# Kernel tuning notes

Measured on AMD Instinct MI355X. Metric: run time of the kernel, lower is better.

Reference implementation:

```python
import jax, jax.numpy as jnp
import numpy as np

N = 100000        # nodes
E = 1600000       # directed edges (before self loops)
F = 128           # input node features
H1, H2, H3 = 64, 32, 16
G = 64            # graphs in batch
EPS = 1e-5
NEG_SLOPE = 0.2


def setup_inputs():
    key = jax.random.key(0)
    ks = jax.random.split(key, 16)
    def rn(k, shape, scale=1.0):
        return jax.random.normal(k, shape, dtype=jnp.float32) * scale
    inp = {}
    inp['x'] = rn(ks[0], (N, F))
    inp['edge_index'] = jax.random.randint(ks[1], (2, E), 0, N)
    inp['batch'] = jnp.sort(jax.random.randint(ks[2], (N,), 0, G))
    dims = [(F, H1), (H1, H2), (H2, H3)]
    i = 3
    for li, (fi, fo) in enumerate(dims, start=1):
        s = 1.0 / np.sqrt(fi)
        kk = jax.random.split(ks[i], 3)
        inp[f'Wl{li}'] = rn(kk[0], (fi, fo), s)
        inp[f'bl{li}'] = jnp.zeros((fo,), jnp.float32)
        inp[f'Wr{li}'] = rn(kk[1], (fi, fo), s)
        inp[f'br{li}'] = jnp.zeros((fo,), jnp.float32)
        inp[f'att{li}'] = rn(kk[2], (fo,), 1.0 / np.sqrt(fo))
        inp[f'bias{li}'] = jnp.zeros((fo,), jnp.float32)
        inp[f'gamma{li}'] = jnp.ones((fo,), jnp.float32)
        inp[f'beta{li}'] = jnp.zeros((fo,), jnp.float32)
        i += 1
    inp['linW'] = rn(ks[i], (H3, 1), 0.25)
    inp['linb'] = jnp.zeros((1,), jnp.float32)
    return inp


def _gatv2(x, Wl, bl, Wr, br, att, bias, src, dst):
    # PyG GATv2Conv, heads=1: e_ij = a^T LeakyReLU(Wl x_j + Wr x_i)
    xl = x @ Wl + bl                         # [N, H] source transform
    xr = x @ Wr + br                         # [N, H] target transform
    e = jax.nn.leaky_relu(xl[src] + xr[dst], NEG_SLOPE) @ att   # [E']
    # numerically stable segment softmax over incoming edges of dst
    emax = jax.ops.segment_max(e, dst, num_segments=N)
    w = jnp.exp(e - emax[dst])
    denom = jax.ops.segment_sum(w, dst, num_segments=N)
    alpha = w / (denom[dst] + 1e-16)         # [E']
    out = jax.ops.segment_sum(alpha[:, None] * xl[src], dst, num_segments=N)
    return out + bias


def _batchnorm(x, gamma, beta):
    mu = jnp.mean(x, axis=0)
    var = jnp.var(x, axis=0)
    return (x - mu) * jax.lax.rsqrt(var + EPS) * gamma + beta


def reference(x, edge_index, batch,
              Wl1, bl1, Wr1, br1, att1, bias1, gamma1, beta1,
              Wl2, bl2, Wr2, br2, att2, bias2, gamma2, beta2,
              Wl3, bl3, Wr3, br3, att3, bias3, gamma3, beta3,
              linW, linb):
    # add self loops once (PyG GATv2Conv default add_self_loops=True)
    loops = jnp.arange(N, dtype=edge_index.dtype)
    src = jnp.concatenate([edge_index[0], loops])
    dst = jnp.concatenate([edge_index[1], loops])

    h = _gatv2(x, Wl1, bl1, Wr1, br1, att1, bias1, src, dst)
    h = jax.nn.relu(_batchnorm(h, gamma1, beta1))
    h = _gatv2(h, Wl2, bl2, Wr2, br2, att2, bias2, src, dst)
    h = jax.nn.relu(_batchnorm(h, gamma2, beta2))
    h = _gatv2(h, Wl3, bl3, Wr3, br3, att3, bias3, src, dst)
    h = jax.nn.relu(_batchnorm(h, gamma3, beta3))

    # global mean pool over graphs
    sums = jax.ops.segment_sum(h, batch, num_segments=G)          # [G, 16]
    cnts = jax.ops.segment_sum(jnp.ones((N,), h.dtype), batch, num_segments=G)
    pooled = sums / jnp.maximum(cnts, 1.0)[:, None]
    return pooled @ linW + linb                                   # [G, 1]
```

## Files before the change

### kernel.cpp

```cpp
#include <hip/hip_runtime.h>
#include <hip/hip_bf16.h>


static constexpr int G_ = 64;

typedef short bfrag __attribute__((ext_vector_type(8)));
typedef float facc  __attribute__((ext_vector_type(4)));

__device__ __forceinline__ float asfloat_(unsigned int u) {
  union { unsigned int i; float f; } c; c.i = u; return c.f;
}
__device__ __forceinline__ float bf2f(unsigned short u) {
  return asfloat_(((unsigned int)u) << 16);
}
__device__ __forceinline__ unsigned short f2bf(float f) {
  union { float f; unsigned int i; } c;
  c.f = f;
  unsigned int r = c.i + 0x7FFFu + ((c.i >> 16) & 1u);
  return (unsigned short)(r >> 16);
}

template <int FPL>
__device__ __forceinline__ void load_bf(const unsigned short* p, float* f) {
  if constexpr (FPL == 8) {
    uint4 q = *reinterpret_cast<const uint4*>(p);
    f[0] = asfloat_(q.x << 16); f[1] = asfloat_(q.x & 0xFFFF0000u);
    f[2] = asfloat_(q.y << 16); f[3] = asfloat_(q.y & 0xFFFF0000u);
    f[4] = asfloat_(q.z << 16); f[5] = asfloat_(q.z & 0xFFFF0000u);
    f[6] = asfloat_(q.w << 16); f[7] = asfloat_(q.w & 0xFFFF0000u);
  } else {
    uint2 q = *reinterpret_cast<const uint2*>(p);
    f[0] = asfloat_(q.x << 16); f[1] = asfloat_(q.x & 0xFFFF0000u);
    f[2] = asfloat_(q.y << 16); f[3] = asfloat_(q.y & 0xFFFF0000u);
  }
}

__global__ __launch_bounds__(256) void pack_all(
    const float* __restrict__ Wl1, const float* __restrict__ Wr1,
    const float* __restrict__ bl1, const float* __restrict__ br1,
    const float* __restrict__ Wl2, const float* __restrict__ Wr2,
    const float* __restrict__ bl2, const float* __restrict__ br2,
    const float* __restrict__ Wl3, const float* __restrict__ Wr3,
    const float* __restrict__ bl3, const float* __restrict__ br3,
    unsigned short* __restrict__ Wt1, float* __restrict__ bc1,
    unsigned short* __restrict__ Wt2, float* __restrict__ bc2,
    unsigned short* __restrict__ Wt3, float* __restrict__ bc3) {
  int i = blockIdx.x * 256 + threadIdx.x;
  if (i < 128 * 128) { int c = i >> 7, k = i & 127;
    Wt1[i] = f2bf((c < 64) ? Wl1[k * 64 + c] : Wr1[k * 64 + (c - 64)]); }
  if (i < 128) bc1[i] = (i < 64) ? bl1[i] : br1[i - 64];
  if (i < 64 * 64) { int c = i >> 6, k = i & 63;
    Wt2[i] = f2bf((c < 32) ? Wl2[k * 32 + c] : Wr2[k * 32 + (c - 32)]); }
  if (i < 64) bc2[i] = (i < 32) ? bl2[i] : br2[i - 32];
  if (i < 32 * 32) { int c = i >> 5, k = i & 31;
    Wt3[i] = f2bf((c < 16) ? Wl3[k * 16 + c] : Wr3[k * 16 + (c - 16)]); }
  if (i < 32) bc3[i] = (i < 16) ? bl3[i] : br3[i - 16];
}

__global__ __launch_bounds__(256) void edge_hist(
    const int* __restrict__ ei, int* __restrict__ deg, int E, int Etot, int N) {
  int p = blockIdx.x & 7;
  int q = blockIdx.x >> 3;
  int nbq = gridDim.x >> 3;
  float scale = 8.0f / (float)N;
  for (int i = q * 256 + threadIdx.x; i < Etot; i += nbq * 256) {
    int dst = (i < E) ? ei[E + i] : (i - E);
    int pp = min((int)((float)dst * scale), 7);
    if (pp == p) atomicAdd(&deg[dst], 1);
  }
}

__global__ __launch_bounds__(256) void scan1(
    const int* __restrict__ deg, int* __restrict__ part, int* __restrict__ bsums, int n) {
  __shared__ int ts[256];
  int t = threadIdx.x, b = blockIdx.x;
  int base = b * 1024 + t * 4;
  int d[4];
#pragma unroll
  for (int q = 0; q < 4; q++) d[q] = (base + q < n) ? deg[base + q] : 0;
  int s = d[0] + d[1] + d[2] + d[3];
  ts[t] = s;
  __syncthreads();
  for (int o = 1; o < 256; o <<= 1) {
    int v = (t >= o) ? ts[t - o] : 0;
    __syncthreads();
    ts[t] += v;
    __syncthreads();
  }
  int incl = ts[t];
  if (t == 255) bsums[b] = incl;
  int run = incl - s;
#pragma unroll
  for (int q = 0; q < 4; q++) {
    if (base + q < n) part[base + q] = run;
    run += d[q];
  }
}

__global__ void scan2(int* bsums, int nb) {
  __shared__ int s[256];
  int t = threadIdx.x;
  int v = (t < nb) ? bsums[t] : 0;
  s[t] = v;
  __syncthreads();
  for (int o = 1; o < 256; o <<= 1) {
    int u = (t >= o) ? s[t - o] : 0;
    __syncthreads();
    s[t] += u;
    __syncthreads();
  }
  if (t < nb) bsums[t] = s[t] - v;
}

__global__ __launch_bounds__(256) void scan3(
    int* __restrict__ rp, int* __restrict__ cur, const int* __restrict__ bsums,
    int n, int Etot) {
  int i = blockIdx.x * 256 + threadIdx.x;
  if (i < n) {
    int v = rp[i] + bsums[i >> 10];
    rp[i] = v; cur[i] = v;
  }
  if (i == 0) rp[n] = Etot;
}

__global__ __launch_bounds__(256) void scatter_edges(
    const int* __restrict__ ei, int* __restrict__ cur, int* __restrict__ ssrc,
    int E, int Etot, int N) {
  int p = blockIdx.x & 7;
  int q = blockIdx.x >> 3;
  int nbq = gridDim.x >> 3;
  float scale = 8.0f / (float)N;
  for (int i = q * 256 + threadIdx.x; i < Etot; i += nbq * 256) {
    int dst = (i < E) ? ei[E + i] : (i - E);
    int pp = min((int)((float)dst * scale), 7);
    if (pp != p) continue;
    int src = (i < E) ? ei[i] : (i - E);
    int pos = atomicAdd(&cur[dst], 1);
    ssrc[pos] = src;
  }
}

template <int FI, int FO, int AMODE>
__global__ __launch_bounds__(256) void gemm_mfma(
    const void* __restrict__ Ain, const float* __restrict__ ssb,
    const unsigned short* __restrict__ Wt, const float* __restrict__ bcat,
    unsigned short* __restrict__ Cb, int N) {
  constexpr int NT = FO / 16;
  constexpr int KS = FI / 32;
  int tid = threadIdx.x;
  int w = tid >> 6;
  int lr = tid & 15;
  int lg = (tid & 63) >> 4;
  int n0 = blockIdx.x * 64;
  int arow = min(n0 + w * 16 + lr, N - 1);

  facc acc[NT];
#pragma unroll
  for (int t = 0; t < NT; t++)
#pragma unroll
    for (int e = 0; e < 4; e++) acc[t][e] = 0.f;

#pragma unroll
  for (int ks = 0; ks < KS; ks++) {
    int k0 = ks * 32 + lg * 8;
    bfrag a;
    if constexpr (AMODE == 0) {
      const unsigned short* Ab = (const unsigned short*)Ain;
      a = *reinterpret_cast<const bfrag*>(&Ab[(size_t)arow * FI + k0]);
    } else {
      const float* Af = (const float*)Ain;
      const float* p = &Af[(size_t)arow * FI + k0];
      float4 lo = *reinterpret_cast<const float4*>(p);
      float4 hi = *reinterpret_cast<const float4*>(p + 4);
      float f[8] = {lo.x, lo.y, lo.z, lo.w, hi.x, hi.y, hi.z, hi.w};
      if constexpr (AMODE == 2) {
        float4 sc0 = *reinterpret_cast<const float4*>(&ssb[k0]);
        float4 sc1 = *reinterpret_cast<const float4*>(&ssb[k0 + 4]);
        float4 sh0 = *reinterpret_cast<const float4*>(&ssb[FI + k0]);
        float4 sh1 = *reinterpret_cast<const float4*>(&ssb[FI + k0 + 4]);
        float sc[8] = {sc0.x, sc0.y, sc0.z, sc0.w, sc1.x, sc1.y, sc1.z, sc1.w};
        float sh[8] = {sh0.x, sh0.y, sh0.z, sh0.w, sh1.x, sh1.y, sh1.z, sh1.w};
#pragma unroll
        for (int e = 0; e < 8; e++) f[e] = fmaxf(fmaf(f[e], sc[e], sh[e]), 0.f);
      }
      union { bfrag v; unsigned short u[8]; } cv;
#pragma unroll
      for (int e = 0; e < 8; e++) cv.u[e] = f2bf(f[e]);
      a = cv.v;
    }
#pragma unroll
    for (int t = 0; t < NT; t++) {
      bfrag b = *reinterpret_cast<const bfrag*>(&Wt[(size_t)(t * 16 + lr) * FI + k0]);
      acc[t] = __builtin_amdgcn_mfma_f32_16x16x32_bf16(a, b, acc[t], 0, 0, 0);
    }
  }

#pragma unroll
  for (int t = 0; t < NT; t++) {
    int col = t * 16 + lr;
    float bias = bcat[col];
#pragma unroll
    for (int r = 0; r < 4; r++) {
      int n = n0 + w * 16 + lg * 4 + r;
      if (n < N) Cb[(size_t)n * FO + col] = f2bf(acc[t][r] + bias);
    }
  }
}

__device__ __forceinline__ float lrelu02(float z) {
  return fmaxf(z, 0.2f * z);
}

template <int H, int FPL, bool UN2>
__global__ __launch_bounds__(256) void gat_agg3(
    const unsigned short* __restrict__ xlr, const float* __restrict__ att,
    const float* __restrict__ bias, const int* __restrict__ rp,
    const int* __restrict__ ssrc, float* __restrict__ out, int N) {
  constexpr int L = H / FPL;
  constexpr int C = 64 / L;
  constexpr int STEP = UN2 ? 2 * C : C;
  int v = blockIdx.x * 4 + (threadIdx.x >> 6);
  if (v >= N) return;
  int lane = threadIdx.x & 63;
  int fl = lane % L;
  int sub = lane / L;

  float xr[FPL], a[FPL];
  load_bf<FPL>(&xlr[(size_t)v * (2 * H) + H + fl * FPL], xr);
#pragma unroll
  for (int e = 0; e < FPL; e += 4) {
    float4 av = *reinterpret_cast<const float4*>(&att[fl * FPL + e]);
    a[e] = av.x; a[e + 1] = av.y; a[e + 2] = av.z; a[e + 3] = av.w;
  }
  int beg = rp[v], end = rp[v + 1];

  float mA = -3.0e38f, dA = 0.f, accA[FPL];
  float mB = -3.0e38f, dB = 0.f, accB[FPL];
#pragma unroll
  for (int e = 0; e < FPL; e++) { accA[e] = 0.f; accB[e] = 0.f; }

  auto edge = [&](int j, float& m, float& d, float (&acc)[FPL]) {
    int u = ssrc[j];
    float xl[FPL];
    load_bf<FPL>(&xlr[(size_t)u * (2 * H) + fl * FPL], xl);
    float t = 0.f;
#pragma unroll
    for (int e = 0; e < FPL; e++) t = fmaf(a[e], lrelu02(xl[e] + xr[e]), t);
#pragma unroll
    for (int o = L / 2; o >= 1; o >>= 1) t += __shfl_xor(t, o);
    float diff = t - m;
    if (diff > 8.f) {
      float sc = __expf(-diff);
      d *= sc;
#pragma unroll
      for (int e = 0; e < FPL; e++) acc[e] *= sc;
      m = t; diff = 0.f;
    }
    float w = __expf(diff);
    d += w;
#pragma unroll
    for (int e = 0; e < FPL; e++) acc[e] = fmaf(w, xl[e], acc[e]);
  };

  for (int j = beg + sub; j < end; j += STEP) {
    edge(j, mA, dA, accA);
    if (UN2) {
      int j2 = j + C;
      if (j2 < end) edge(j2, mB, dB, accB);
    }
  }

  if (UN2) {
    float mn = fmaxf(mA, mB);
    float s1 = __expf(mA - mn), s2 = __expf(mB - mn);
    dA = dA * s1 + dB * s2;
#pragma unroll
    for (int e = 0; e < FPL; e++) accA[e] = accA[e] * s1 + accB[e] * s2;
    mA = mn;
  }

#pragma unroll
  for (int o = L; o < 64; o <<= 1) {
    float mo = __shfl_xor(mA, o);
    float d2 = __shfl_xor(dA, o);
    float ao[FPL];
#pragma unroll
    for (int e = 0; e < FPL; e++) ao[e] = __shfl_xor(accA[e], o);
    float mn = fmaxf(mA, mo);
    float s1 = __expf(mA - mn), s2 = __expf(mo - mn);
    dA = dA * s1 + d2 * s2;
#pragma unroll
    for (int e = 0; e < FPL; e++) accA[e] = accA[e] * s1 + ao[e] * s2;
    mA = mn;
  }

  if (lane < L) {
    float inv = 1.f / (dA + 1e-16f);
#pragma unroll
    for (int e = 0; e < FPL; e += 4) {
      float4 b4 = *reinterpret_cast<const float4*>(&bias[fl * FPL + e]);
      float4 o4 = make_float4(fmaf(accA[e + 0], inv, b4.x),
                              fmaf(accA[e + 1], inv, b4.y),
                              fmaf(accA[e + 2], inv, b4.z),
                              fmaf(accA[e + 3], inv, b4.w));
      *reinterpret_cast<float4*>(&out[(size_t)v * H + fl * FPL + e]) = o4;
    }
  }
}

template <int H>
__global__ __launch_bounds__(256) void bn_stats(
    const float* __restrict__ X, float* __restrict__ stats, int N) {
  __shared__ float ls[256], ls2[256];
  int tid = threadIdx.x;
  int h = tid % H;
  constexpr int RPB = 256 / H;
  int r0 = blockIdx.x * RPB + tid / H;
  float s = 0.f, s2 = 0.f;
  for (int n = r0; n < N; n += gridDim.x * RPB) {
    float val = X[(size_t)n * H + h];
    s += val; s2 += val * val;
  }
  ls[tid] = s; ls2[tid] = s2;
  __syncthreads();
  if (tid < H) {
    for (int g = 1; g < RPB; g++) { s += ls[tid + g * H]; s2 += ls2[tid + g * H]; }
    atomicAdd(&stats[h], s);
    atomicAdd(&stats[H + h], s2);
  }
}

__global__ void bn_finalize(
    const float* __restrict__ stats, const float* __restrict__ gamma,
    const float* __restrict__ beta, float* __restrict__ ss, int H, int N) {
  int h = threadIdx.x;
  if (h < H) {
    float mean = stats[h] / (float)N;
    float var = stats[H + h] / (float)N - mean * mean;
    float istd = rsqrtf(var + 1e-5f);
    float sc = gamma[h] * istd;
    ss[h] = sc;
    ss[H + h] = beta[h] - mean * sc;
  }
}

__global__ __launch_bounds__(256) void pool_kernel(
    const float* __restrict__ X, const float* __restrict__ ss,
    const int* __restrict__ batch, float* __restrict__ pool,
    float* __restrict__ cnt, int N) {
  __shared__ float lp[G_ * 16];
  __shared__ float lc[G_];
  int tid = threadIdx.x;
  for (int j = tid; j < G_ * 16; j += 256) lp[j] = 0.f;
  if (tid < G_) lc[tid] = 0.f;
  __syncthreads();
  int tot = N * 16;
  for (int i = blockIdx.x * 256 + tid; i < tot; i += gridDim.x * 256) {
    int n = i >> 4, h = i & 15;
    int g = batch[n];
    float t = X[i] * ss[h] + ss[16 + h];
    t = (t > 0.f) ? t : 0.f;
    atomicAdd(&lp[g * 16 + h], t);
    if (h == 0) atomicAdd(&lc[g], 1.0f);
  }
  __syncthreads();
  for (int j = tid; j < G_ * 16; j += 256) atomicAdd(&pool[j], lp[j]);
  if (tid < G_) atomicAdd(&cnt[tid], lc[tid]);
}

__global__ void final_linear(
    const float* __restrict__ pool, const float* __restrict__ cnt,
    const float* __restrict__ linW, const float* __restrict__ linb,
    float* __restrict__ out) {
  int g = threadIdx.x;
  if (g < G_) {
    float c = fmaxf(cnt[g], 1.0f);
    float acc = 0.f;
    for (int h = 0; h < 16; h++) acc += (pool[g * 16 + h] / c) * linW[h];
    out[g] = acc + linb[0];
  }
}

extern "C" void kernel_launch(void* const* d_in, const int* in_sizes, int n_in,
                              void* d_out, int out_size, void* d_ws, size_t ws_size,
                              hipStream_t stream) {
  const float* x = (const float*)d_in[0];
  const int* ei = (const int*)d_in[1];
  const int* batch = (const int*)d_in[2];
  const int N = in_sizes[0] / 128;
  const int E = in_sizes[1] / 2;
  const int Etot = E + N;

  char* wsb = (char*)d_ws;
  size_t off = 0;
  auto alloc = [&](size_t bytes) -> void* {
    void* p = wsb + off;
    off += (bytes + 255) & ~(size_t)255;
    return p;
  };
  unsigned short* R1b = (unsigned short*)alloc((size_t)128 * N * 2);
  float* R2 = (float*)alloc((size_t)64 * N * 4);
  int* row_ptr = (int*)alloc((size_t)(N + 1) * 4);
  int* cursor = (int*)alloc((size_t)N * 4);
  int* bsums = (int*)alloc(4096);
  int* ssrc = (int*)alloc((size_t)Etot * 4);
  unsigned short* Wt1 = (unsigned short*)alloc(16384 * 2);
  float* bc1 = (float*)alloc(128 * 4);
  unsigned short* Wt2 = (unsigned short*)alloc(4096 * 2);
  float* bc2 = (float*)alloc(64 * 4);
  unsigned short* Wt3 = (unsigned short*)alloc(1024 * 2);
  float* bc3 = (float*)alloc(32 * 4);
  float* ss = (float*)alloc(256 * 4);
  size_t zelems = (size_t)N + 3 * 128 + G_ * 16 + G_;
  char* zb = (char*)alloc(zelems * 4);
  int* deg = (int*)zb;
  float* stats1 = (float*)(zb + (size_t)N * 4);
  float* stats2 = stats1 + 128;
  float* stats3 = stats2 + 128;
  float* pool = stats3 + 128;
  float* cnt = pool + G_ * 16;

  const float* Wl1 = (const float*)d_in[3];  const float* bl1 = (const float*)d_in[4];
  const float* Wr1 = (const float*)d_in[5];  const float* br1 = (const float*)d_in[6];
  const float* att1 = (const float*)d_in[7]; const float* bias1 = (const float*)d_in[8];
  const float* g1 = (const float*)d_in[9];   const float* b1 = (const float*)d_in[10];
  const float* Wl2 = (const float*)d_in[11]; const float* bl2 = (const float*)d_in[12];
  const float* Wr2 = (const float*)d_in[13]; const float* br2 = (const float*)d_in[14];
  const float* att2 = (const float*)d_in[15]; const float* bias2 = (const float*)d_in[16];
  const float* g2 = (const float*)d_in[17];  const float* b2 = (const float*)d_in[18];
  const float* Wl3 = (const float*)d_in[19]; const float* bl3 = (const float*)d_in[20];
  const float* Wr3 = (const float*)d_in[21]; const float* br3 = (const float*)d_in[22];
  const float* att3 = (const float*)d_in[23]; const float* bias3 = (const float*)d_in[24];
  const float* g3 = (const float*)d_in[25];  const float* b3 = (const float*)d_in[26];
  const float* linW = (const float*)d_in[27]; const float* linb = (const float*)d_in[28];
  float* out = (float*)d_out;

  int nb = (N + 1023) / 1024;
  int nnodeblk = (N + 3) / 4;
  int ngemm = (N + 63) / 64;

  pack_all<<<64, 256, 0, stream>>>(Wl1, Wr1, bl1, br1, Wl2, Wr2, bl2, br2,
                                   Wl3, Wr3, bl3, br3, Wt1, bc1, Wt2, bc2, Wt3, bc3);
  hipMemsetAsync(zb, 0, zelems * 4, stream);

  edge_hist<<<4096, 256, 0, stream>>>(ei, deg, E, Etot, N);
  scan1<<<nb, 256, 0, stream>>>(deg, row_ptr, bsums, N);
  scan2<<<1, 256, 0, stream>>>(bsums, nb);
  scan3<<<(N + 255) / 256, 256, 0, stream>>>(row_ptr, cursor, bsums, N, Etot);
  scatter_edges<<<4096, 256, 0, stream>>>(ei, cursor, ssrc, E, Etot, N);

  gemm_mfma<128, 128, 1><<<ngemm, 256, 0, stream>>>(x, nullptr, Wt1, bc1, R1b, N);
  gat_agg3<64, 8, true><<<nnodeblk, 256, 0, stream>>>(R1b, att1, bias1, row_ptr, ssrc, R2, N);
  bn_stats<64><<<512, 256, 0, stream>>>(R2, stats1, N);
  bn_finalize<<<1, 64, 0, stream>>>(stats1, g1, b1, ss, 64, N);

  gemm_mfma<64, 64, 2><<<ngemm, 256, 0, stream>>>(R2, ss, Wt2, bc2, R1b, N);
  gat_agg3<32, 8, true><<<nnodeblk, 256, 0, stream>>>(R1b, att2, bias2, row_ptr, ssrc, R2, N);
  bn_stats<32><<<512, 256, 0, stream>>>(R2, stats2, N);
  bn_finalize<<<1, 64, 0, stream>>>(stats2, g2, b2, ss, 32, N);

  gemm_mfma<32, 32, 2><<<ngemm, 256, 0, stream>>>(R2, ss, Wt3, bc3, R1b, N);
  gat_agg3<16, 4, false><<<nnodeblk, 256, 0, stream>>>(R1b, att3, bias3, row_ptr, ssrc, R2, N);
  bn_stats<16><<<512, 256, 0, stream>>>(R2, stats3, N);
  bn_finalize<<<1, 64, 0, stream>>>(stats3, g3, b3, ss, 16, N);

  pool_kernel<<<2048, 256, 0, stream>>>(R2, ss, batch, pool, cnt, N);
  final_linear<<<1, 64, 0, stream>>>(pool, cnt, linW, linb, out);
}
```

Before: 538.8 us.

## Split XL/XR into separate buffers and use 4 features per lane in aggregation

The GEMM now writes the source transform XL and the target transform XR to two separate bf16 arrays instead of one interleaved [N,2H] buffer. The per-edge gather of a source row then reads a contiguous H-wide row, which packs more useful rows per cache line for the random gather. The aggregation kernel also moves from 8 to 4 features per lane, so more edges are processed in parallel per wavefront with fewer registers per lane. The cost is more shuffle-reduction steps per edge and smaller 8-byte loads in place of 16-byte loads.

```diff
diff --git a/kernel.cpp b/kernel.cpp
--- a/kernel.cpp
+++ b/kernel.cpp
@@ -9,9 +9,6 @@
 
 __device__ __forceinline__ float asfloat_(unsigned int u) {
   union { unsigned int i; float f; } c; c.i = u; return c.f;
-}
-__device__ __forceinline__ float bf2f(unsigned short u) {
-  return asfloat_(((unsigned int)u) << 16);
 }
 __device__ __forceinline__ unsigned short f2bf(float f) {
   union { float f; unsigned int i; } c;
@@ -20,19 +17,10 @@
   return (unsigned short)(r >> 16);
 }
 
-template <int FPL>
-__device__ __forceinline__ void load_bf(const unsigned short* p, float* f) {
-  if constexpr (FPL == 8) {
-    uint4 q = *reinterpret_cast<const uint4*>(p);
-    f[0] = asfloat_(q.x << 16); f[1] = asfloat_(q.x & 0xFFFF0000u);
-    f[2] = asfloat_(q.y << 16); f[3] = asfloat_(q.y & 0xFFFF0000u);
-    f[4] = asfloat_(q.z << 16); f[5] = asfloat_(q.z & 0xFFFF0000u);
-    f[6] = asfloat_(q.w << 16); f[7] = asfloat_(q.w & 0xFFFF0000u);
-  } else {
-    uint2 q = *reinterpret_cast<const uint2*>(p);
-    f[0] = asfloat_(q.x << 16); f[1] = asfloat_(q.x & 0xFFFF0000u);
-    f[2] = asfloat_(q.y << 16); f[3] = asfloat_(q.y & 0xFFFF0000u);
-  }
+__device__ __forceinline__ void load_bf4(const unsigned short* p, float* f) {
+  uint2 q = *reinterpret_cast<const uint2*>(p);
+  f[0] = asfloat_(q.x << 16); f[1] = asfloat_(q.x & 0xFFFF0000u);
+  f[2] = asfloat_(q.y << 16); f[3] = asfloat_(q.y & 0xFFFF0000u);
 }
 
 __global__ __launch_bounds__(256) void pack_all(
@@ -144,9 +132,10 @@
 __global__ __launch_bounds__(256) void gemm_mfma(
     const void* __restrict__ Ain, const float* __restrict__ ssb,
     const unsigned short* __restrict__ Wt, const float* __restrict__ bcat,
-    unsigned short* __restrict__ Cb, int N) {
+    unsigned short* __restrict__ XL, unsigned short* __restrict__ XR, int N) {
   constexpr int NT = FO / 16;
   constexpr int KS = FI / 32;
+  constexpr int H = FO / 2;
   int tid = threadIdx.x;
   int w = tid >> 6;
   int lr = tid & 15;
@@ -199,10 +188,12 @@
   for (int t = 0; t < NT; t++) {
     int col = t * 16 + lr;
     float bias = bcat[col];
+    unsigned short* dstbuf = (t < NT / 2) ? XL : XR;
+    int cc = (t < NT / 2) ? col : (col - H);
 #pragma unroll
     for (int r = 0; r < 4; r++) {
       int n = n0 + w * 16 + lg * 4 + r;
-      if (n < N) Cb[(size_t)n * FO + col] = f2bf(acc[t][r] + bias);
+      if (n < N) dstbuf[(size_t)n * H + cc] = f2bf(acc[t][r] + bias);
     }
   }
 }
@@ -211,12 +202,13 @@
   return fmaxf(z, 0.2f * z);
 }
 
-template <int H, int FPL, bool UN2>
-__global__ __launch_bounds__(256) void gat_agg3(
-    const unsigned short* __restrict__ xlr, const float* __restrict__ att,
-    const float* __restrict__ bias, const int* __restrict__ rp,
-    const int* __restrict__ ssrc, float* __restrict__ out, int N) {
-  constexpr int L = H / FPL;
+template <int H, bool UN2>
+__global__ __launch_bounds__(256) void gat_agg4(
+    const unsigned short* __restrict__ XL, const unsigned short* __restrict__ XR,
+    const float* __restrict__ att, const float* __restrict__ bias,
+    const int* __restrict__ rp, const int* __restrict__ ssrc,
+    float* __restrict__ out, int N) {
+  constexpr int L = H / 4;
   constexpr int C = 64 / L;
   constexpr int STEP = UN2 ? 2 * C : C;
   int v = blockIdx.x * 4 + (threadIdx.x >> 6);
@@ -225,27 +217,22 @@
   int fl = lane % L;
   int sub = lane / L;
 
-  float xr[FPL], a[FPL];
-  load_bf<FPL>(&xlr[(size_t)v * (2 * H) + H + fl * FPL], xr);
-#pragma unroll
-  for (int e = 0; e < FPL; e += 4) {
-    float4 av = *reinterpret_cast<const float4*>(&att[fl * FPL + e]);
-    a[e] = av.x; a[e + 1] = av.y; a[e + 2] = av.z; a[e + 3] = av.w;
-  }
+  float xr[4];
+  load_bf4(&XR[(size_t)v * H + fl * 4], xr);
+  const float4 a4 = *reinterpret_cast<const float4*>(&att[fl * 4]);
   int beg = rp[v], end = rp[v + 1];
 
-  float mA = -3.0e38f, dA = 0.f, accA[FPL];
-  float mB = -3.0e38f, dB = 0.f, accB[FPL];
-#pragma unroll
-  for (int e = 0; e < FPL; e++) { accA[e] = 0.f; accB[e] = 0.f; }
-
-  auto edge = [&](int j, float& m, float& d, float (&acc)[FPL]) {
+  float mA = -3.0e38f, dA = 0.f, accA[4] = {0.f, 0.f, 0.f, 0.f};
+  float mB = -3.0e38f, dB = 0.f, accB[4] = {0.f, 0.f, 0.f, 0.f};
+
+  auto edge = [&](int j, float& m, float& d, float (&acc)[4]) {
     int u = ssrc[j];
-    float xl[FPL];
-    load_bf<FPL>(&xlr[(size_t)u * (2 * H) + fl * FPL], xl);
-    float t = 0.f;
-#pragma unroll
-    for (int e = 0; e < FPL; e++) t = fmaf(a[e], lrelu02(xl[e] + xr[e]), t);
+    float xl[4];
+    load_bf4(&XL[(size_t)u * H + fl * 4], xl);
+    float t = a4.x * lrelu02(xl[0] + xr[0]);
+    t = fmaf(a4.y, lrelu02(xl[1] + xr[1]), t);
+    t = fmaf(a4.z, lrelu02(xl[2] + xr[2]), t);
+    t = fmaf(a4.w, lrelu02(xl[3] + xr[3]), t);
 #pragma unroll
     for (int o = L / 2; o >= 1; o >>= 1) t += __shfl_xor(t, o);
     float diff = t - m;
@@ -253,13 +240,13 @@
       float sc = __expf(-diff);
       d *= sc;
 #pragma unroll
-      for (int e = 0; e < FPL; e++) acc[e] *= sc;
+      for (int e = 0; e < 4; e++) acc[e] *= sc;
       m = t; diff = 0.f;
     }
     float w = __expf(diff);
     d += w;
 #pragma unroll
-    for (int e = 0; e < FPL; e++) acc[e] = fmaf(w, xl[e], acc[e]);
+    for (int e = 0; e < 4; e++) acc[e] = fmaf(w, xl[e], acc[e]);
   };
 
   for (int j = beg + sub; j < end; j += STEP) {
@@ -275,7 +262,7 @@
     float s1 = __expf(mA - mn), s2 = __expf(mB - mn);
     dA = dA * s1 + dB * s2;
 #pragma unroll
-    for (int e = 0; e < FPL; e++) accA[e] = accA[e] * s1 + accB[e] * s2;
+    for (int e = 0; e < 4; e++) accA[e] = accA[e] * s1 + accB[e] * s2;
     mA = mn;
   }
 
@@ -283,28 +270,26 @@
   for (int o = L; o < 64; o <<= 1) {
     float mo = __shfl_xor(mA, o);
     float d2 = __shfl_xor(dA, o);
-    float ao[FPL];
-#pragma unroll
-    for (int e = 0; e < FPL; e++) ao[e] = __shfl_xor(accA[e], o);
+    float a0 = __shfl_xor(accA[0], o);
+    float a1 = __shfl_xor(accA[1], o);
+    float a2 = __shfl_xor(accA[2], o);
+    float a3 = __shfl_xor(accA[3], o);
     float mn = fmaxf(mA, mo);
     float s1 = __expf(mA - mn), s2 = __expf(mo - mn);
     dA = dA * s1 + d2 * s2;
-#pragma unroll
-    for (int e = 0; e < FPL; e++) accA[e] = accA[e] * s1 + ao[e] * s2;
+    accA[0] = accA[0] * s1 + a0 * s2;
+    accA[1] = accA[1] * s1 + a1 * s2;
+    accA[2] = accA[2] * s1 + a2 * s2;
+    accA[3] = accA[3] * s1 + a3 * s2;
     mA = mn;
   }
 
   if (lane < L) {
     float inv = 1.f / (dA + 1e-16f);
-#pragma unroll
-    for (int e = 0; e < FPL; e += 4) {
-      float4 b4 = *reinterpret_cast<const float4*>(&bias[fl * FPL + e]);
-      float4 o4 = make_float4(fmaf(accA[e + 0], inv, b4.x),
-                              fmaf(accA[e + 1], inv, b4.y),
-                              fmaf(accA[e + 2], inv, b4.z),
-                              fmaf(accA[e + 3], inv, b4.w));
-      *reinterpret_cast<float4*>(&out[(size_t)v * H + fl * FPL + e]) = o4;
-    }
+    const float4 b4 = *reinterpret_cast<const float4*>(&bias[fl * 4]);
+    float4 o4 = make_float4(fmaf(accA[0], inv, b4.x), fmaf(accA[1], inv, b4.y),
+                            fmaf(accA[2], inv, b4.z), fmaf(accA[3], inv, b4.w));
+    *reinterpret_cast<float4*>(&out[(size_t)v * H + fl * 4]) = o4;
   }
 }
 
@@ -398,7 +383,8 @@
     off += (bytes + 255) & ~(size_t)255;
     return p;
   };
-  unsigned short* R1b = (unsigned short*)alloc((size_t)128 * N * 2);
+  unsigned short* XLb = (unsigned short*)alloc((size_t)64 * N * 2);
+  unsigned short* XRb = (unsigned short*)alloc((size_t)64 * N * 2);
   float* R2 = (float*)alloc((size_t)64 * N * 4);
   int* row_ptr = (int*)alloc((size_t)(N + 1) * 4);
   int* cursor = (int*)alloc((size_t)N * 4);
@@ -449,18 +435,18 @@
   scan3<<<(N + 255) / 256, 256, 0, stream>>>(row_ptr, cursor, bsums, N, Etot);
   scatter_edges<<<4096, 256, 0, stream>>>(ei, cursor, ssrc, E, Etot, N);
 
-  gemm_mfma<128, 128, 1><<<ngemm, 256, 0, stream>>>(x, nullptr, Wt1, bc1, R1b, N);
-  gat_agg3<64, 8, true><<<nnodeblk, 256, 0, stream>>>(R1b, att1, bias1, row_ptr, ssrc, R2, N);
+  gemm_mfma<128, 128, 1><<<ngemm, 256, 0, stream>>>(x, nullptr, Wt1, bc1, XLb, XRb, N);
+  gat_agg4<64, true><<<nnodeblk, 256, 0, stream>>>(XLb, XRb, att1, bias1, row_ptr, ssrc, R2, N);
   bn_stats<64><<<512, 256, 0, stream>>>(R2, stats1, N);
   bn_finalize<<<1, 64, 0, stream>>>(stats1, g1, b1, ss, 64, N);
 
-  gemm_mfma<64, 64, 2><<<ngemm, 256, 0, stream>>>(R2, ss, Wt2, bc2, R1b, N);
-  gat_agg3<32, 8, true><<<nnodeblk, 256, 0, stream>>>(R1b, att2, bias2, row_ptr, ssrc, R2, N);
+  gemm_mfma<64, 64, 2><<<ngemm, 256, 0, stream>>>(R2, ss, Wt2, bc2, XLb, XRb, N);
+  gat_agg4<32, true><<<nnodeblk, 256, 0, stream>>>(XLb, XRb, att2, bias2, row_ptr, ssrc, R2, N);
   bn_stats<32><<<512, 256, 0, stream>>>(R2, stats2, N);
   bn_finalize<<<1, 64, 0, stream>>>(stats2, g2, b2, ss, 32, N);
 
-  gemm_mfma<32, 32, 2><<<ngemm, 256, 0, stream>>>(R2, ss, Wt3, bc3, R1b, N);
-  gat_agg3<16, 4, false><<<nnodeblk, 256, 0, stream>>>(R1b, att3, bias3, row_ptr, ssrc, R2, N);
+  gemm_mfma<32, 32, 2><<<ngemm, 256, 0, stream>>>(R2, ss, Wt3, bc3, XLb, XRb, N);
+  gat_agg4<16, false><<<nnodeblk, 256, 0, stream>>>(XLb, XRb, att3, bias3, row_ptr, ssrc, R2, N);
   bn_stats<16><<<512, 256, 0, stream>>>(R2, stats3, N);
   bn_finalize<<<1, 64, 0, stream>>>(stats3, g3, b3, ss, 16, N);
 
```

Measured after the change: 510.1 us. 5.3% less time.
